# Optimization experiments

Hardware: AMD Instinct MI355X
Metric: run time of the kernel (lower is better)

The kernel has to match this reference:

```python
import jax, jax.numpy as jnp
import numpy as np

N, E, B = 50000, 400000, 50
F_IN, HID, HEADS, F_OUT = 128, 32, 8, 64
HC = HID * HEADS  # 256


def gat_conv(x, src, dst, W, a_s, a_d, b, n):
    """PyG-style GATConv (concat=True, negative_slope=0.2), inference mode."""
    H, C = a_s.shape
    h = (x @ W).reshape(n, H, C)                       # [N,H,C]
    alpha_s = (h * a_s).sum(-1)                        # [N,H]
    alpha_d = (h * a_d).sum(-1)                        # [N,H]
    logits = jax.nn.leaky_relu(alpha_s[src] + alpha_d[dst], 0.2)  # [E,H]
    m = jax.ops.segment_max(logits, dst, num_segments=n)
    m = jnp.where(jnp.isfinite(m), m, 0.0)
    e = jnp.exp(logits - m[dst])
    den = jax.ops.segment_sum(e, dst, num_segments=n)
    alpha = e / (den[dst] + 1e-16)                     # segment softmax over dst
    out = jax.ops.segment_sum(h[src] * alpha[:, :, None], dst, num_segments=n)
    return out.reshape(n, H * C) + b


def setup_inputs() -> dict:
    key = jax.random.key(0)
    ks = jax.random.split(key, 24)
    s = 0.1
    inp = {
        "x": jax.random.normal(ks[0], (N, F_IN), jnp.float32),
        "edge_index": jax.random.randint(ks[1], (2, E), 0, N),
        "batch": jnp.sort(jax.random.randint(ks[2], (N,), 0, B)),
        "W1": jax.random.normal(ks[3], (F_IN, HC), jnp.float32) * s,
        "a_src1": jax.random.normal(ks[4], (HEADS, HID), jnp.float32) * s,
        "a_dst1": jax.random.normal(ks[5], (HEADS, HID), jnp.float32) * s,
        "b1": jnp.zeros((HC,), jnp.float32),
        "W2": jax.random.normal(ks[6], (HC, HC), jnp.float32) * s,
        "a_src2": jax.random.normal(ks[7], (1, HC), jnp.float32) * s,
        "a_dst2": jax.random.normal(ks[8], (1, HC), jnp.float32) * s,
        "b2": jnp.zeros((HC,), jnp.float32),
        "W3": jax.random.normal(ks[9], (HC, HC), jnp.float32) * s,
        "a_src3": jax.random.normal(ks[10], (1, HC), jnp.float32) * s,
        "a_dst3": jax.random.normal(ks[11], (1, HC), jnp.float32) * s,
        "b3": jnp.zeros((HC,), jnp.float32),
        "W4": jax.random.normal(ks[12], (HC, F_OUT), jnp.float32) * s,
        "a_src4": jax.random.normal(ks[13], (1, F_OUT), jnp.float32) * s,
        "a_dst4": jax.random.normal(ks[14], (1, F_OUT), jnp.float32) * s,
        "b4": jnp.zeros((F_OUT,), jnp.float32),
        "Wl": jax.random.normal(ks[15], (F_OUT, 1), jnp.float32) * s,
        "bl": jnp.zeros((1,), jnp.float32),
    }
    return inp


def reference(x, edge_index, batch, W1, a_src1, a_dst1, b1, W2, a_src2, a_dst2, b2,
              W3, a_src3, a_dst3, b3, W4, a_src4, a_dst4, b4, Wl, bl):
    n = x.shape[0]
    loop = jnp.arange(n)
    src = jnp.concatenate([edge_index[0], loop])  # add self loops (PyG default)
    dst = jnp.concatenate([edge_index[1], loop])
    x = jax.nn.elu(gat_conv(x, src, dst, W1, a_src1, a_dst1, b1, n))
    x = jax.nn.elu(gat_conv(x, src, dst, W2, a_src2, a_dst2, b2, n))
    x = jax.nn.elu(gat_conv(x, src, dst, W3, a_src3, a_dst3, b3, n))
    x_gat = gat_conv(x, src, dst, W4, a_src4, a_dst4, b4, n)
    # to_dense_batch(x_gat, batch).mean(dim=1): sum per graph / max graph size
    counts = jax.ops.segment_sum(jnp.ones((n,), x_gat.dtype), batch, num_segments=B)
    max_nodes = counts.max()
    pooled = jax.ops.segment_sum(x_gat, batch, num_segments=B) / max_nodes  # [B,F_OUT]
    return pooled @ Wl + bl  # [B,1]
```

## Files before the change

kernel.cpp:

```cpp
#include <hip/hip_runtime.h>
#include <math.h>


typedef __attribute__((ext_vector_type(8))) short short8;
typedef __attribute__((ext_vector_type(4))) float f32x4;

__device__ __forceinline__ unsigned short f2bf(float f) {
  unsigned int u = __builtin_bit_cast(unsigned int, f);
  unsigned int r = u + 0x7FFFu + ((u >> 16) & 1u);
  return (unsigned short)(r >> 16);
}
__device__ __forceinline__ float bf2f(unsigned short h) {
  unsigned int u = ((unsigned int)h) << 16;
  return __builtin_bit_cast(float, u);
}
__device__ __forceinline__ unsigned short f2h(float f) {
  _Float16 h = (_Float16)f;
  return __builtin_bit_cast(unsigned short, h);
}
__device__ __forceinline__ float h2f(unsigned short u) {
  return (float)__builtin_bit_cast(_Float16, u);
}

__device__ __forceinline__ void gload16(const unsigned short* g, unsigned short* l) {
  __builtin_amdgcn_global_load_lds(
      (const __attribute__((address_space(1))) void*)g,
      (__attribute__((address_space(3))) void*)l, 16, 0, 0);
}

template<int H>
__global__ __launch_bounds__(256) void k_gemm_mfma(
    const unsigned short* __restrict__ A2, const unsigned short* __restrict__ Wt,
    unsigned short* __restrict__ C, const float* __restrict__ avec_s,
    const float* __restrict__ avec_d, float* __restrict__ outS,
    float* __restrict__ outD, int M, int Kb, int Nc)
{
  __shared__ unsigned short lds[16384];
  unsigned short* As = lds;
  unsigned short* Bs = lds + 8192;
  const int tid = threadIdx.x;
  const int w = tid >> 6, l = tid & 63;
  const int row0 = blockIdx.x * 128, col0 = blockIdx.y * 128;
  const int wr = w >> 1, wc = w & 1;
  const int fr = l & 15, kg = l >> 4;
  const int xr = (fr & 7) << 4;
  const int sK = 2 * Kb;
  const int csrc = 8 * ((l & 7) ^ ((l >> 3) & 7));
  const int rstage = w * 32 + (l >> 3);

  f32x4 acc[4][4];
  #pragma unroll
  for (int i = 0; i < 4; i++)
    #pragma unroll
    for (int j = 0; j < 4; j++) acc[i][j] = (f32x4){0.f, 0.f, 0.f, 0.f};

  for (int kp = 0; kp < sK; kp += 64) {
    #pragma unroll
    for (int i = 0; i < 4; i++) {
      int r = rstage + i * 8;
      gload16(&A2[(size_t)(row0 + r) * sK + (kp + csrc)], &As[w * 2048 + i * 512]);
      gload16(&Wt[(size_t)(col0 + r) * sK + (kp + csrc)], &Bs[w * 2048 + i * 512]);
    }
    __syncthreads();
    #pragma unroll
    for (int kk = 0; kk < 2; kk++) {
      short8 a[4], b[4];
      #pragma unroll
      for (int mi = 0; mi < 4; mi++) {
        int r = wr * 64 + mi * 16 + fr;
        int off = r * 128 + ((kk * 64 + kg * 16) ^ xr);
        a[mi] = *(const short8*)((const char*)As + off);
      }
      #pragma unroll
      for (int ni = 0; ni < 4; ni++) {
        int c = wc * 64 + ni * 16 + fr;
        int off = c * 128 + ((kk * 64 + kg * 16) ^ xr);
        b[ni] = *(const short8*)((const char*)Bs + off);
      }
      #pragma unroll
      for (int mi = 0; mi < 4; mi++)
        #pragma unroll
        for (int ni = 0; ni < 4; ni++)
          acc[mi][ni] = __builtin_amdgcn_mfma_f32_16x16x32_bf16(
              a[mi], b[ni], acc[mi][ni], 0, 0, 0);
    }
    __syncthreads();
  }

  #pragma unroll
  for (int mi = 0; mi < 4; mi++)
    #pragma unroll
    for (int ni = 0; ni < 4; ni++)
      #pragma unroll
      for (int rr = 0; rr < 4; rr++) {
        int row = wr * 64 + mi * 16 + kg * 4 + rr;
        int c = wc * 64 + ni * 16 + fr;
        int sc = c ^ (((row >> 1) & 7) << 3);
        lds[row * 128 + sc] = f2h(acc[mi][ni][rr]);
      }
  __syncthreads();

  constexpr int RW = (H == 8) ? 4 : 16;
  const int Ch = Nc / H;
  const int rbase = tid >> 4;
  const int cc = tid & 15;
  const int c0 = cc * 8;
  const int gc0 = col0 + c0;
  float as8[8], ad8[8];
  #pragma unroll
  for (int j = 0; j < 8; j++) {
    bool ok = (gc0 + j) < Nc;
    as8[j] = ok ? avec_s[gc0 + j] : 0.f;
    ad8[j] = ok ? avec_d[gc0 + j] : 0.f;
  }
  #pragma unroll
  for (int i = 0; i < 8; i++) {
    int row = rbase + i * 16;
    int gr = row0 + row;
    int scc = c0 ^ (((row >> 1) & 7) << 3);
    short8 cv = *(const short8*)&lds[row * 128 + scc];
    if (gr < M && gc0 < Nc)
      *(short8*)&C[(size_t)gr * Nc + gc0] = cv;
    float ps = 0.f, pd = 0.f;
    #pragma unroll
    for (int j = 0; j < 8; j++) {
      float cf = h2f((unsigned short)cv[j]);
      ps = fmaf(cf, as8[j], ps);
      pd = fmaf(cf, ad8[j], pd);
    }
    #pragma unroll
    for (int off = 1; off < RW; off <<= 1) {
      ps += __shfl_xor(ps, off);
      pd += __shfl_xor(pd, off);
    }
    if ((tid & (RW - 1)) == 0 && gr < M) {
      int head = gc0 / Ch;
      atomicAdd(&outS[gr * H + head], ps);
      atomicAdd(&outD[gr * H + head], pd);
    }
  }
}

__global__ __launch_bounds__(256) void k_packX(const float* __restrict__ x,
    unsigned short* __restrict__ A2, int N, int Mpad)
{
  int row = blockIdx.x * 8 + (threadIdx.x >> 5);
  int c = (threadIdx.x & 31) * 4;
  if (row >= Mpad) return;
  float4 v = make_float4(0.f, 0.f, 0.f, 0.f);
  if (row < N) v = *(const float4*)&x[(size_t)row * 128 + c];
  float f[4] = {v.x, v.y, v.z, v.w};
  unsigned short hi[4], lo[4];
  #pragma unroll
  for (int i = 0; i < 4; i++) {
    hi[i] = f2bf(f[i]);
    lo[i] = f2bf(f[i] - bf2f(hi[i]));
  }
  size_t base = (size_t)row * 256 + c;
  *(uint2*)&A2[base] = make_uint2((unsigned)hi[0] | ((unsigned)hi[1] << 16),
                                  (unsigned)hi[2] | ((unsigned)hi[3] << 16));
  *(uint2*)&A2[base + 128] = make_uint2((unsigned)lo[0] | ((unsigned)lo[1] << 16),
                                        (unsigned)lo[2] | ((unsigned)lo[3] << 16));
}

__global__ void k_packW(const float* __restrict__ W, unsigned short* __restrict__ Wt,
                        int K, int NC, int NCPAD)
{
  int idx = blockIdx.x * 256 + threadIdx.x;
  int K2 = 2 * K;
  if (idx >= NCPAD * K2) return;
  int c = idx / K2, kp = idx % K2;
  unsigned short o = 0;
  if (c < NC) o = f2bf(W[(size_t)(kp % K) * NC + c]);
  Wt[(size_t)c * K2 + kp] = o;
}

template<int H, int HC, int ELU, int SPLIT>
__global__ __launch_bounds__(256) void k_aggregate(const unsigned short* __restrict__ h,
    const float* __restrict__ as, const float* __restrict__ ad,
    const int* __restrict__ rowptr, const int* __restrict__ col,
    const float* __restrict__ bias, float* __restrict__ xout,
    unsigned short* __restrict__ a2out, int N)
{
  constexpr int VEC = HC / 64;
  constexpr int C = HC / H;
  constexpr int CH = (H == 8) ? 8 : 64;
  int wave = threadIdx.x >> 6, lane = threadIdx.x & 63;
  int row = blockIdx.x * 4 + wave;
  if (row >= N) return;
  const int cb = lane * VEC;
  const int hdg = cb / C;
  int s0 = rowptr[row], s1 = rowptr[row + 1];

  float adv = (H == 8) ? ad[row * 8 + (lane & 7)] : ad[row];
  float den = 0.f;
  float acc[VEC];
  #pragma unroll
  for (int v = 0; v < VEC; v++) acc[v] = 0.f;

  for (int base = s0; base < s1; base += CH) {
    int cnt = min(CH, s1 - base);
    int eo = (H == 8) ? (lane >> 3) : lane;
    bool valid = eo < cnt;
    int s = col[valid ? (base + eo) : (s1 - 1)];
    float lg = ((H == 8) ? as[s * 8 + (lane & 7)] : as[s]) + adv;
    lg = fmaxf(lg, 0.2f * lg);
    float wgt = valid ? __expf(lg) : 0.f;
    float d = wgt;
    if (H == 8) {
      d += __shfl_xor(d, 8); d += __shfl_xor(d, 16); d += __shfl_xor(d, 32);
    } else {
      #pragma unroll
      for (int off = 1; off < 64; off <<= 1) d += __shfl_xor(d, off);
    }
    den += d;
    #pragma unroll 2
    for (int j = 0; j < cnt; j++) {
      int sj = __shfl(s, (H == 8) ? (j * 8) : j);
      float wj = __shfl(wgt, (H == 8) ? (j * 8 + hdg) : j);
      if constexpr (VEC == 4) {
        uint2 raw = *(const uint2*)&h[(size_t)sj * HC + cb];
        acc[0] = fmaf(wj, h2f((unsigned short)(raw.x & 0xFFFF)), acc[0]);
        acc[1] = fmaf(wj, h2f((unsigned short)(raw.x >> 16)),    acc[1]);
        acc[2] = fmaf(wj, h2f((unsigned short)(raw.y & 0xFFFF)), acc[2]);
        acc[3] = fmaf(wj, h2f((unsigned short)(raw.y >> 16)),    acc[3]);
      } else {
        acc[0] = fmaf(wj, h2f(h[(size_t)sj * HC + cb]), acc[0]);
      }
    }
  }
  if (H == 8) den = __shfl(den, hdg);
  float inv = 1.f / (den + 1e-16f);
  float o[VEC];
  #pragma unroll
  for (int v = 0; v < VEC; v++) {
    float t = acc[v] * inv + bias[cb + v];
    if (ELU) t = t > 0.f ? t : expm1f(t);
    o[v] = t;
  }
  if constexpr (SPLIT) {
    unsigned short hi[4], lo[4];
    #pragma unroll
    for (int v = 0; v < 4; v++) {
      hi[v] = f2bf(o[v]);
      lo[v] = f2bf(o[v] - bf2f(hi[v]));
    }
    size_t base = (size_t)row * (2 * HC) + cb;
    *(uint2*)&a2out[base] = make_uint2((unsigned)hi[0] | ((unsigned)hi[1] << 16),
                                       (unsigned)hi[2] | ((unsigned)hi[3] << 16));
    *(uint2*)&a2out[base + HC] = make_uint2((unsigned)lo[0] | ((unsigned)lo[1] << 16),
                                            (unsigned)lo[2] | ((unsigned)lo[3] << 16));
  } else if constexpr (VEC == 4) {
    *(float4*)&xout[(size_t)row * HC + cb] = make_float4(o[0], o[1], o[2], o[3]);
  } else {
    xout[(size_t)row * HC + cb] = o[0];
  }
}

__global__ void k_init(int* deg, float* pool, unsigned short* A2, int N, int B,
                       int Mpad) {
  int i = blockIdx.x * 256 + threadIdx.x;
  if (i < N) deg[i] = 1;
  if (i < B * 64) pool[i] = 0.f;
  int padn = (Mpad - N) * 512;
  if (i < padn) A2[(size_t)N * 512 + i] = 0;
}

__global__ void k_deg(const int* __restrict__ ei, int* deg, int E) {
  int e = blockIdx.x * 256 + threadIdx.x;
  if (e < E) atomicAdd(&deg[ei[E + e]], 1);
}

__global__ void k_counts(const int* __restrict__ bat, int* cnt, int N, int B) {
  int b = threadIdx.x;
  if (b >= B) return;
  int lo0 = 0, hi0 = N;
  while (lo0 < hi0) { int mid = (lo0 + hi0) >> 1; if (bat[mid] < b) lo0 = mid + 1; else hi0 = mid; }
  int lo1 = lo0, hi1 = N;
  while (lo1 < hi1) { int mid = (lo1 + hi1) >> 1; if (bat[mid] < b + 1) lo1 = mid + 1; else hi1 = mid; }
  cnt[b] = lo1 - lo0;
}

__global__ __launch_bounds__(256) void k_scan1(const int* __restrict__ deg,
                                               int* csum, int N, int chunk) {
  int bid = blockIdx.x, t = threadIdx.x;
  int lo = bid * chunk, hi = min(lo + chunk, N);
  int s = 0;
  for (int i = lo + t; i < hi; i += 256) s += deg[i];
  #pragma unroll
  for (int off = 32; off; off >>= 1) s += __shfl_xor(s, off);
  __shared__ int sh[4];
  if ((t & 63) == 0) sh[t >> 6] = s;
  __syncthreads();
  if (t == 0) csum[bid] = sh[0] + sh[1] + sh[2] + sh[3];
}

__global__ __launch_bounds__(256) void k_scan2(const int* __restrict__ csum,
                                               int* coff) {
  __shared__ int s[256];
  int t = threadIdx.x;
  int v0 = csum[t];
  s[t] = v0;
  for (int off = 1; off < 256; off <<= 1) {
    __syncthreads();
    int v = (t >= off) ? s[t - off] : 0;
    __syncthreads();
    s[t] += v;
  }
  __syncthreads();
  coff[t] = s[t] - v0;
}

__global__ __launch_bounds__(256) void k_scan3(const int* __restrict__ deg,
    const int* __restrict__ coff, int* rowptr, int* cursor, int N, int chunk) {
  __shared__ int s[256];
  int bid = blockIdx.x, t = threadIdx.x;
  int i = bid * chunk + t;
  int v = (t < chunk && i < N) ? deg[i] : 0;
  s[t] = v;
  for (int off = 1; off < 256; off <<= 1) {
    __syncthreads();
    int x = (t >= off) ? s[t - off] : 0;
    __syncthreads();
    s[t] += x;
  }
  __syncthreads();
  int excl = s[t] - v + coff[bid];
  if (t < chunk && i < N) {
    rowptr[i] = excl;
    cursor[i] = excl;
    if (i == N - 1) rowptr[N] = excl + v;
  }
}

__global__ void k_scatter(const int* __restrict__ ei, int* cursor, int* col,
                          int E, int N) {
  int idx = blockIdx.x * 256 + threadIdx.x;
  if (idx >= E + N) return;
  int s, d;
  if (idx < E) { s = ei[idx]; d = ei[E + idx]; }
  else         { s = d = idx - E; }
  int pos = atomicAdd(&cursor[d], 1);
  col[pos] = s;
}

__global__ __launch_bounds__(256) void k_pool(const float* __restrict__ xg,
    const int* __restrict__ bat, float* pool, int N) {
  int lane = threadIdx.x & 63, w = threadIdx.x >> 6;
  int base = (blockIdx.x * 4 + w) * 16;
  if (base >= N) return;
  int end = min(base + 16, N);
  float local = 0.f;
  int curb = bat[base];
  for (int n = base; n < end; n++) {
    int b = bat[n];
    if (b != curb) {
      atomicAdd(&pool[curb * 64 + lane], local);
      local = 0.f; curb = b;
    }
    local += xg[(size_t)n * 64 + lane];
  }
  atomicAdd(&pool[curb * 64 + lane], local);
}

__global__ void k_final(const float* __restrict__ pool, const int* __restrict__ cnt,
    const float* __restrict__ Wl, const float* __restrict__ bl,
    float* __restrict__ out, int B) {
  int lane = threadIdx.x;
  int c = (lane < B) ? cnt[lane] : 0;
  #pragma unroll
  for (int off = 32; off; off >>= 1) c = max(c, __shfl_xor(c, off));
  float invm = 1.f / (float)c;
  float wl = Wl[lane];
  for (int b = 0; b < B; b++) {
    float ps = pool[b * 64 + lane] * wl;
    #pragma unroll
    for (int off = 32; off; off >>= 1) ps += __shfl_xor(ps, off);
    if (lane == 0) out[b] = ps * invm + bl[0];
  }
}

extern "C" void kernel_launch(void* const* d_in, const int* in_sizes, int n_in,
                              void* d_out, int out_size, void* d_ws, size_t ws_size,
                              hipStream_t stream)
{
  (void)n_in; (void)ws_size;
  const float* x   = (const float*)d_in[0];
  const int*   ei  = (const int*)d_in[1];
  const int*   bat = (const int*)d_in[2];
  const float* W1  = (const float*)d_in[3];
  const float* as1 = (const float*)d_in[4];
  const float* ad1 = (const float*)d_in[5];
  const float* b1  = (const float*)d_in[6];
  const float* W2  = (const float*)d_in[7];
  const float* as2 = (const float*)d_in[8];
  const float* ad2 = (const float*)d_in[9];
  const float* b2  = (const float*)d_in[10];
  const float* W3  = (const float*)d_in[11];
  const float* as3 = (const float*)d_in[12];
  const float* ad3 = (const float*)d_in[13];
  const float* b3  = (const float*)d_in[14];
  const float* W4  = (const float*)d_in[15];
  const float* as4 = (const float*)d_in[16];
  const float* ad4 = (const float*)d_in[17];
  const float* b4  = (const float*)d_in[18];
  const float* Wl  = (const float*)d_in[19];
  const float* bl  = (const float*)d_in[20];
  float* out = (float*)d_out;

  const int N = in_sizes[0] / 128;
  const int E = in_sizes[1] / 2;
  const int B = out_size;
  const int Mpad = ((N + 127) / 128) * 128;

  char* p = (char*)d_ws;
  auto alloc = [&](size_t bytes) -> void* {
    void* r = (void*)p;
    p += ((bytes + 255) & ~(size_t)255);
    return r;
  };
  unsigned short* A2 = (unsigned short*)alloc((size_t)Mpad * 512 * 2);
  unsigned short* hbuf = (unsigned short*)alloc((size_t)N * 256 * 2);
  unsigned short* w2t1 = (unsigned short*)alloc((size_t)256 * 512 * 2);
  unsigned short* w2t2 = (unsigned short*)alloc((size_t)256 * 512 * 2);
  unsigned short* w2t3 = (unsigned short*)alloc((size_t)256 * 512 * 2);
  unsigned short* w2t4 = (unsigned short*)alloc((size_t)128 * 512 * 2);
  float* aAll  = (float*)alloc((size_t)N * 22 * 4);
  float* aSb   = aAll;
  float* aDb   = aAll + (size_t)N * 11;
  int*   deg   = (int*)alloc((size_t)N * 4);
  int*   rowptr= (int*)alloc((size_t)(N + 1) * 4);
  int*   cursor= (int*)alloc((size_t)N * 4);
  int*   col   = (int*)alloc((size_t)(E + N) * 4);
  int*   csum  = (int*)alloc(256 * 4);
  int*   coff  = (int*)alloc(256 * 4);
  float* pool  = (float*)alloc((size_t)B * 64 * 4);
  int*   cnt   = (int*)alloc((size_t)B * 4);
  float* xpool = (float*)A2;

  const int chunk = (N + 255) / 256;
  dim3 T(256);

  k_init<<<dim3((N + 255) / 256), T, 0, stream>>>(deg, pool, A2, N, B, Mpad);
  k_deg<<<dim3((E + 255) / 256), T, 0, stream>>>(ei, deg, E);
  k_counts<<<dim3(1), dim3(64), 0, stream>>>(bat, cnt, N, B);
  k_scan1<<<dim3(256), T, 0, stream>>>(deg, csum, N, chunk);
  k_scan2<<<dim3(1), T, 0, stream>>>(csum, coff);
  k_scan3<<<dim3(256), T, 0, stream>>>(deg, coff, rowptr, cursor, N, chunk);
  k_scatter<<<dim3((E + N + 255) / 256), T, 0, stream>>>(ei, cursor, col, E, N);
  hipMemsetAsync(aAll, 0, (size_t)N * 22 * 4, stream);

  k_packX<<<dim3(Mpad / 8), T, 0, stream>>>(x, A2, N, Mpad);
  k_packW<<<dim3((256 * 256 + 255) / 256), T, 0, stream>>>(W1, w2t1, 128, 256, 256);
  k_packW<<<dim3((256 * 512 + 255) / 256), T, 0, stream>>>(W2, w2t2, 256, 256, 256);
  k_packW<<<dim3((256 * 512 + 255) / 256), T, 0, stream>>>(W3, w2t3, 256, 256, 256);
  k_packW<<<dim3((128 * 512 + 255) / 256), T, 0, stream>>>(W4, w2t4, 256, 64, 128);

  dim3 nwav((N + 3) / 4);
  dim3 g2(Mpad / 128, 2), g1(Mpad / 128, 1);

  float* aS1 = aSb;                 float* aD1 = aDb;
  float* aS2 = aSb + (size_t)N * 8; float* aD2 = aDb + (size_t)N * 8;
  float* aS3 = aSb + (size_t)N * 9; float* aD3 = aDb + (size_t)N * 9;
  float* aS4 = aSb + (size_t)N * 10;float* aD4 = aDb + (size_t)N * 10;

  k_gemm_mfma<8><<<g2, T, 0, stream>>>(A2, w2t1, hbuf, as1, ad1, aS1, aD1, N, 128, 256);
  k_aggregate<8, 256, 1, 1><<<nwav, T, 0, stream>>>(hbuf, aS1, aD1, rowptr, col, b1,
                                                    nullptr, A2, N);
  k_gemm_mfma<1><<<g2, T, 0, stream>>>(A2, w2t2, hbuf, as2, ad2, aS2, aD2, N, 256, 256);
  k_aggregate<1, 256, 1, 1><<<nwav, T, 0, stream>>>(hbuf, aS2, aD2, rowptr, col, b2,
                                                    nullptr, A2, N);
  k_gemm_mfma<1><<<g2, T, 0, stream>>>(A2, w2t3, hbuf, as3, ad3, aS3, aD3, N, 256, 256);
  k_aggregate<1, 256, 1, 1><<<nwav, T, 0, stream>>>(hbuf, aS3, aD3, rowptr, col, b3,
                                                    nullptr, A2, N);
  k_gemm_mfma<1><<<g1, T, 0, stream>>>(A2, w2t4, hbuf, as4, ad4, aS4, aD4, N, 256, 64);
  k_aggregate<1, 64, 0, 0><<<nwav, T, 0, stream>>>(hbuf, aS4, aD4, rowptr, col, b4,
                                                   xpool, nullptr, N);

  k_pool<<<dim3((N + 63) / 64), T, 0, stream>>>(xpool, bat, pool, N);
  k_final<<<dim3(1), dim3(64), 0, stream>>>(pool, cnt, Wl, bl, out, B);
}
```

Measured before the change: 454.9 us.

## Widen aggregation gathers with multi-edge lanes and halve GEMM row tile

The aggregation kernel now stages per-edge source indices and softmax weights in LDS. Each lane loads 8 fp16 channels at once, so several edges are processed in parallel per wave, followed by a cross-lane reduction. This is meant to cut per-edge shuffle overhead and issue wider, fewer gather instructions. Separately, the MFMA GEMM row tile is halved to 64, which doubles the grid for better CU occupancy at the cost of more B-tile reloads.

```diff
diff --git a/kernel.cpp b/kernel.cpp
--- a/kernel.cpp
+++ b/kernel.cpp
@@ -35,39 +35,43 @@
     const float* __restrict__ avec_d, float* __restrict__ outS,
     float* __restrict__ outD, int M, int Kb, int Nc)
 {
-  __shared__ unsigned short lds[16384];
+  __shared__ unsigned short lds[12288];
   unsigned short* As = lds;
-  unsigned short* Bs = lds + 8192;
+  unsigned short* Bs = lds + 4096;
   const int tid = threadIdx.x;
   const int w = tid >> 6, l = tid & 63;
-  const int row0 = blockIdx.x * 128, col0 = blockIdx.y * 128;
+  const int row0 = blockIdx.x * 64, col0 = blockIdx.y * 128;
   const int wr = w >> 1, wc = w & 1;
   const int fr = l & 15, kg = l >> 4;
   const int xr = (fr & 7) << 4;
   const int sK = 2 * Kb;
   const int csrc = 8 * ((l & 7) ^ ((l >> 3) & 7));
-  const int rstage = w * 32 + (l >> 3);
-
-  f32x4 acc[4][4];
-  #pragma unroll
-  for (int i = 0; i < 4; i++)
+  const int lrow = l >> 3;
+
+  f32x4 acc[2][4];
+  #pragma unroll
+  for (int i = 0; i < 2; i++)
     #pragma unroll
     for (int j = 0; j < 4; j++) acc[i][j] = (f32x4){0.f, 0.f, 0.f, 0.f};
 
   for (int kp = 0; kp < sK; kp += 64) {
     #pragma unroll
+    for (int i = 0; i < 2; i++) {
+      int q = w * 2 + i;
+      gload16(&A2[(size_t)(row0 + q * 8 + lrow) * sK + (kp + csrc)], &As[q * 512]);
+    }
+    #pragma unroll
     for (int i = 0; i < 4; i++) {
-      int r = rstage + i * 8;
-      gload16(&A2[(size_t)(row0 + r) * sK + (kp + csrc)], &As[w * 2048 + i * 512]);
-      gload16(&Wt[(size_t)(col0 + r) * sK + (kp + csrc)], &Bs[w * 2048 + i * 512]);
+      int q = w * 4 + i;
+      gload16(&Wt[(size_t)(col0 + q * 8 + lrow) * sK + (kp + csrc)], &Bs[q * 512]);
     }
     __syncthreads();
     #pragma unroll
     for (int kk = 0; kk < 2; kk++) {
-      short8 a[4], b[4];
-      #pragma unroll
-      for (int mi = 0; mi < 4; mi++) {
-        int r = wr * 64 + mi * 16 + fr;
+      short8 a[2], b[4];
+      #pragma unroll
+      for (int mi = 0; mi < 2; mi++) {
+        int r = wr * 32 + mi * 16 + fr;
         int off = r * 128 + ((kk * 64 + kg * 16) ^ xr);
         a[mi] = *(const short8*)((const char*)As + off);
       }
@@ -78,7 +82,7 @@
         b[ni] = *(const short8*)((const char*)Bs + off);
       }
       #pragma unroll
-      for (int mi = 0; mi < 4; mi++)
+      for (int mi = 0; mi < 2; mi++)
         #pragma unroll
         for (int ni = 0; ni < 4; ni++)
           acc[mi][ni] = __builtin_amdgcn_mfma_f32_16x16x32_bf16(
@@ -88,12 +92,12 @@
   }
 
   #pragma unroll
-  for (int mi = 0; mi < 4; mi++)
+  for (int mi = 0; mi < 2; mi++)
     #pragma unroll
     for (int ni = 0; ni < 4; ni++)
       #pragma unroll
       for (int rr = 0; rr < 4; rr++) {
-        int row = wr * 64 + mi * 16 + kg * 4 + rr;
+        int row = wr * 32 + mi * 16 + kg * 4 + rr;
         int c = wc * 64 + ni * 16 + fr;
         int sc = c ^ (((row >> 1) & 7) << 3);
         lds[row * 128 + sc] = f2h(acc[mi][ni][rr]);
@@ -114,7 +118,7 @@
     ad8[j] = ok ? avec_d[gc0 + j] : 0.f;
   }
   #pragma unroll
-  for (int i = 0; i < 8; i++) {
+  for (int i = 0; i < 4; i++) {
     int row = rbase + i * 16;
     int gr = row0 + row;
     int scc = c0 ^ (((row >> 1) & 7) << 3);
@@ -182,21 +186,26 @@
     const float* __restrict__ bias, float* __restrict__ xout,
     unsigned short* __restrict__ a2out, int N)
 {
-  constexpr int VEC = HC / 64;
+  constexpr int LPR = HC / 8;
+  constexpr int EPI = 64 / LPR;
   constexpr int C = HC / H;
   constexpr int CH = (H == 8) ? 8 : 64;
+  __shared__ float wlds[4][CH * H];
+  __shared__ int   slds[4][CH];
   int wave = threadIdx.x >> 6, lane = threadIdx.x & 63;
   int row = blockIdx.x * 4 + wave;
   if (row >= N) return;
-  const int cb = lane * VEC;
-  const int hdg = cb / C;
+  const int g  = lane / LPR;
+  const int li = lane % LPR;
+  const int cb = li * 8;
+  const int hd2 = cb / C;
   int s0 = rowptr[row], s1 = rowptr[row + 1];
 
   float adv = (H == 8) ? ad[row * 8 + (lane & 7)] : ad[row];
   float den = 0.f;
-  float acc[VEC];
-  #pragma unroll
-  for (int v = 0; v < VEC; v++) acc[v] = 0.f;
+  float acc[8];
+  #pragma unroll
+  for (int v = 0; v < 8; v++) acc[v] = 0.f;
 
   for (int base = s0; base < s1; base += CH) {
     int cnt = min(CH, s1 - base);
@@ -207,53 +216,61 @@
     lg = fmaxf(lg, 0.2f * lg);
     float wgt = valid ? __expf(lg) : 0.f;
     float d = wgt;
-    if (H == 8) {
+    if constexpr (H == 8) {
       d += __shfl_xor(d, 8); d += __shfl_xor(d, 16); d += __shfl_xor(d, 32);
+      wlds[wave][(lane >> 3) * 8 + (lane & 7)] = wgt;
+      if ((lane & 7) == 0) slds[wave][lane >> 3] = s;
     } else {
       #pragma unroll
       for (int off = 1; off < 64; off <<= 1) d += __shfl_xor(d, off);
+      wlds[wave][lane] = wgt;
+      slds[wave][lane] = s;
     }
     den += d;
+    asm volatile("s_waitcnt lgkmcnt(0)" ::: "memory");
+    __builtin_amdgcn_sched_barrier(0);
     #pragma unroll 2
-    for (int j = 0; j < cnt; j++) {
-      int sj = __shfl(s, (H == 8) ? (j * 8) : j);
-      float wj = __shfl(wgt, (H == 8) ? (j * 8 + hdg) : j);
-      if constexpr (VEC == 4) {
-        uint2 raw = *(const uint2*)&h[(size_t)sj * HC + cb];
-        acc[0] = fmaf(wj, h2f((unsigned short)(raw.x & 0xFFFF)), acc[0]);
-        acc[1] = fmaf(wj, h2f((unsigned short)(raw.x >> 16)),    acc[1]);
-        acc[2] = fmaf(wj, h2f((unsigned short)(raw.y & 0xFFFF)), acc[2]);
-        acc[3] = fmaf(wj, h2f((unsigned short)(raw.y >> 16)),    acc[3]);
-      } else {
-        acc[0] = fmaf(wj, h2f(h[(size_t)sj * HC + cb]), acc[0]);
+    for (int j = 0; j < cnt; j += EPI) {
+      int e = j + g;
+      int sj = slds[wave][e];
+      float wj = wlds[wave][e * H + hd2];
+      uint4 raw = *(const uint4*)&h[(size_t)sj * HC + cb];
+      unsigned int rw[4] = {raw.x, raw.y, raw.z, raw.w};
+      #pragma unroll
+      for (int q = 0; q < 4; q++) {
+        acc[2*q]   = fmaf(wj, h2f((unsigned short)(rw[q] & 0xFFFF)), acc[2*q]);
+        acc[2*q+1] = fmaf(wj, h2f((unsigned short)(rw[q] >> 16)),    acc[2*q+1]);
       }
     }
   }
-  if (H == 8) den = __shfl(den, hdg);
-  float inv = 1.f / (den + 1e-16f);
-  float o[VEC];
-  #pragma unroll
-  for (int v = 0; v < VEC; v++) {
-    float t = acc[v] * inv + bias[cb + v];
-    if (ELU) t = t > 0.f ? t : expm1f(t);
-    o[v] = t;
-  }
-  if constexpr (SPLIT) {
-    unsigned short hi[4], lo[4];
-    #pragma unroll
-    for (int v = 0; v < 4; v++) {
-      hi[v] = f2bf(o[v]);
-      lo[v] = f2bf(o[v] - bf2f(hi[v]));
-    }
-    size_t base = (size_t)row * (2 * HC) + cb;
-    *(uint2*)&a2out[base] = make_uint2((unsigned)hi[0] | ((unsigned)hi[1] << 16),
-                                       (unsigned)hi[2] | ((unsigned)hi[3] << 16));
-    *(uint2*)&a2out[base + HC] = make_uint2((unsigned)lo[0] | ((unsigned)lo[1] << 16),
-                                            (unsigned)lo[2] | ((unsigned)lo[3] << 16));
-  } else if constexpr (VEC == 4) {
-    *(float4*)&xout[(size_t)row * HC + cb] = make_float4(o[0], o[1], o[2], o[3]);
-  } else {
-    xout[(size_t)row * HC + cb] = o[0];
+  if constexpr (H == 8) den = __shfl(den, hd2);
+  #pragma unroll
+  for (int off = LPR; off < 64; off <<= 1)
+    #pragma unroll
+    for (int v = 0; v < 8; v++) acc[v] += __shfl_xor(acc[v], off);
+  if (g == 0) {
+    float inv = 1.f / (den + 1e-16f);
+    float o[8];
+    #pragma unroll
+    for (int v = 0; v < 8; v++) {
+      float t = acc[v] * inv + bias[cb + v];
+      if (ELU) t = t > 0.f ? t : expm1f(t);
+      o[v] = t;
+    }
+    if constexpr (SPLIT) {
+      short8 hi8, lo8;
+      #pragma unroll
+      for (int v = 0; v < 8; v++) {
+        unsigned short hi = f2bf(o[v]);
+        unsigned short lo = f2bf(o[v] - bf2f(hi));
+        hi8[v] = (short)hi; lo8[v] = (short)lo;
+      }
+      *(short8*)&a2out[(size_t)row * (2 * HC) + cb] = hi8;
+      *(short8*)&a2out[(size_t)row * (2 * HC) + HC + cb] = lo8;
+    } else {
+      *(float4*)&xout[(size_t)row * HC + cb] = make_float4(o[0], o[1], o[2], o[3]);
+      *(float4*)&xout[(size_t)row * HC + cb + 4] = make_float4(o[4], o[5], o[6], o[7]);
+    }
   }
 }
 
@@ -457,7 +474,7 @@
   k_packW<<<dim3((128 * 512 + 255) / 256), T, 0, stream>>>(W4, w2t4, 256, 64, 128);
 
   dim3 nwav((N + 3) / 4);
-  dim3 g2(Mpad / 128, 2), g1(Mpad / 128, 1);
+  dim3 g2(Mpad / 64, 2), g1(Mpad / 64, 1);
 
   float* aS1 = aSb;                 float* aD1 = aDb;
   float* aS2 = aSb + (size_t)N * 8; float* aD2 = aDb + (size_t)N * 8;
```

Result: no change. 458.7 us (+0.8%).
